# Kernel tuning notes

Measured on AMD Instinct MI355X. Metric: run time of the kernel, lower is better.

Reference implementation:

```python
import jax, jax.numpy as jnp
import numpy as np

LAYER_START = 4
WIN = 2          # context_window_size (over the LAYER axis)
NORM_EPS = 1e-12 # F.normalize eps
COS_EPS = 1e-8   # cosine_similarity eps


def _alpha_for_k(sf, k, nlay):
    """Alignment/novelty weights for layer k. sf: [B, Ttok, Lay, H].
    Mirrors torch: left = tf[k-w:k] (empty when k<w due to python slicing),
    right = tf[k+1:k+w+1], self row last; QR of window_matrix.T."""
    left = list(range(k - WIN, k)) if k >= WIN else []
    right = list(range(k + 1, min(k + WIN + 1, nlay)))
    rows = left + right + [k]
    m = len(rows)  # 3..5
    W = sf[:, :, jnp.array(rows), :]          # [B,T,m,H]
    A = jnp.swapaxes(W, -1, -2)               # [B,T,H,m]  (window_matrix.T)
    _, R = jnp.linalg.qr(A)                   # reduced: R [B,T,m,m]
    r = R[..., :, -1]                         # [B,T,m]
    Rsub = R[..., :-1, :-1]                   # [B,T,m-1,m-1]
    coln = Rsub / jnp.maximum(jnp.linalg.norm(Rsub, axis=-2, keepdims=True), NORM_EPS)
    row_mean = jnp.mean(coln, axis=-1)        # mean over columns -> [B,T,m-1]
    align = jnp.sum(row_mean * R[..., :-1, -1], axis=-1) / jnp.linalg.norm(r[..., :-1], axis=-1)
    align = 1.0 / (align * m * 2)
    novelty = jnp.abs(r[..., -1]) / jnp.linalg.norm(r, axis=-1)
    return align, novelty


def wk_forward(all_hidden_states, attention_mask):
    # [NL,B,T,H] -> [B, Lay, T, H] after layer_start slice
    emb = jnp.transpose(all_hidden_states, (1, 0, 2, 3))[:, LAYER_START:, :, :]
    B, Lay, T, H = emb.shape
    ntok = T - 1  # attention_mask is all-ones: unmask_num = sum(mask) - 1
    sf = jnp.transpose(emb[:, :, :ntok, :], (0, 2, 1, 3))  # [B,Ttok,Lay,H]
    aligns, novs = [], []
    for k in range(Lay):  # small fixed loop over 9 layers
        a, n = _alpha_for_k(sf, k, Lay)
        aligns.append(a)
        novs.append(n)
    align = jnp.stack(aligns, axis=-1)  # [B,Ttok,Lay]
    nov = jnp.stack(novs, axis=-1)
    align = align / jnp.sum(align, axis=-1, keepdims=True)
    nov = nov / jnp.sum(nov, axis=-1, keepdims=True)
    alpha = align + nov
    alpha = alpha / jnp.sum(alpha, axis=-1, keepdims=True)
    token_emb = jnp.einsum('btl,btlh->bth', alpha, sf)  # unify_token output per token
    # unify_sentence: per-token variance (unbiased) of consecutive-layer cosine sims
    a, b = sf[:, :, 1:, :], sf[:, :, :-1, :]
    num = jnp.sum(a * b, axis=-1)
    den = jnp.maximum(jnp.linalg.norm(a, axis=-1) * jnp.linalg.norm(b, axis=-1), COS_EPS)
    sims = num / den                              # [B,Ttok,Lay-1]
    var_tok = jnp.var(sims, axis=-1, ddof=1)      # torch.var default unbiased
    var_tok = var_tok / jnp.sum(var_tok, axis=-1, keepdims=True)
    return jnp.einsum('bt,bth->bh', var_tok, token_emb)  # [B,H]


def setup_inputs() -> dict:
    key = jax.random.key(0)
    NL, B, T, H = 13, 8, 512, 768
    all_hidden_states = jax.random.normal(key, (NL, B, T, H), dtype=jnp.float32)
    attention_mask = jnp.ones((B, T), dtype=jnp.int32)
    return {"all_hidden_states": all_hidden_states, "attention_mask": attention_mask}


def reference(all_hidden_states, attention_mask):
    return wk_forward(all_hidden_states, attention_mask)
```

## Files before the change

kernel.cpp:

```cpp
#include <hip/hip_runtime.h>
#include <math.h>

#define B_DIM 8
#define T_DIM 512
#define H_DIM 768
#define NTOK 511
#define NLAY 9
#define LAYER_START 4
#define NBAND 35
#define TCHUNK 128

__device__ float g_part[B_DIM * TCHUNK * H_DIM];
__device__ float g_varp[B_DIM * TCHUNK];

#define BOFF(d) ((d)*9 - (d) * ((d)-1) / 2)

__global__ __launch_bounds__(256, 4) void wk_a(const float* __restrict__ ahs) {
  const int chunk = blockIdx.x;
  const int b = blockIdx.y;
  const int wave = threadIdx.x >> 6;
  const int lane = threadIdx.x & 63;
  const int t_raw = chunk * 4 + wave;
  const bool active = (t_raw < NTOK);
  const int t = active ? t_raw : (NTOK - 1);

  __shared__ float sG[4][36];
  __shared__ float lds_out[4][H_DIM];
  __shared__ float lds_var[4];

  const size_t LSTR = (size_t)B_DIM * T_DIM * H_DIM;
  const float* lay0 =
      ahs + (size_t)LAYER_START * LSTR + ((size_t)b * T_DIM + t) * H_DIM;

  float g[NBAND];
#pragma unroll
  for (int p = 0; p < NBAND; ++p) g[p] = 0.f;

#pragma unroll 1
  for (int s = 0; s < 3; ++s) {
    const float* p0 = lay0 + s * 256 + lane * 4;
    float4 vs[NLAY];
#pragma unroll
    for (int l = 0; l < NLAY; ++l)
      vs[l] = *reinterpret_cast<const float4*>(p0 + (size_t)l * LSTR);
#pragma unroll
    for (int d = 0; d <= 4; ++d) {
#pragma unroll
      for (int i = 0; i + d < NLAY; ++i) {
        const float4 x = vs[i], y = vs[i + d];
        g[BOFF(d) + i] += x.x * y.x + x.y * y.y + x.z * y.z + x.w * y.w;
      }
    }
  }

#pragma unroll
  for (int off = 32; off > 0; off >>= 1) {
#pragma unroll
    for (int p = 0; p < NBAND; ++p) g[p] += __shfl_xor(g[p], off, 64);
  }

  if (lane == 0) {
#pragma unroll
    for (int p = 0; p < NBAND; ++p) sG[wave][p] = g[p];
  }
  __syncthreads();

  const int k = lane < NLAY ? lane : NLAY - 1;
  const int nl = (k >= 2) ? 2 : 0;
  const int nrr = (NLAY - 1 - k) < 2 ? (NLAY - 1 - k) : 2;
  const int m = nl + nrr + 1;

  auto rowf = [&](int i) -> int {
    return (i < nl) ? (k - 2 + i) : ((i < nl + nrr) ? (k + 1 + i - nl) : k);
  };
  auto GK = [&](int i, int j) -> float {
    int a = rowf(i), c = rowf(j);
    int lo = a < c ? a : c;
    int d = (a < c ? c : a) - lo;
    return sG[wave][d * 9 - d * (d - 1) / 2 + lo];
  };

  float R[5][5];
#pragma unroll
  for (int j = 0; j < 5; ++j)
#pragma unroll
    for (int i = 0; i < 5; ++i) R[i][j] = 0.f;

#pragma unroll
  for (int j = 0; j < 5; ++j) {
    if (j < m) {
#pragma unroll
      for (int i = 0; i < 5; ++i) {
        if (i < j) {
          float s = GK(i, j);
#pragma unroll
          for (int p = 0; p < 4; ++p)
            if (p < i) s -= R[p][i] * R[p][j];
          R[i][j] = s / R[i][i];
        }
      }
      float sjj = GK(j, j);
#pragma unroll
      for (int p = 0; p < 4; ++p)
        if (p < j) sjj -= R[p][j] * R[p][j];
      R[j][j] = sqrtf(fmaxf(sjj, 0.f));
    }
  }

  float r[5];
#pragma unroll
  for (int i = 0; i < 5; ++i)
    r[i] = (m == 3) ? R[i][2] : ((m == 4) ? R[i][3] : R[i][4]);

  float rowmean[4] = {0.f, 0.f, 0.f, 0.f};
#pragma unroll
  for (int j = 0; j < 4; ++j) {
    if (j < m - 1) {
      float cn = 0.f;
#pragma unroll
      for (int i = 0; i < 4; ++i)
        if (i <= j) cn += R[i][j] * R[i][j];
      cn = fmaxf(sqrtf(cn), 1e-12f);
      float inv = 1.f / cn;
#pragma unroll
      for (int i = 0; i < 4; ++i)
        if (i < m - 1) rowmean[i] += R[i][j] * inv;
    }
  }

  const float inv_m1 = 1.f / (float)(m - 1);
  float dotv = 0.f, nrm2 = 0.f;
#pragma unroll
  for (int i = 0; i < 4; ++i) {
    if (i < m - 1) {
      dotv += (rowmean[i] * inv_m1) * r[i];
      nrm2 += r[i] * r[i];
    }
  }
  float align_raw = dotv / sqrtf(nrm2);
  float align_v = 1.f / (align_raw * (float)m * 2.f);
  float rlast = (m == 3) ? r[2] : ((m == 4) ? r[3] : r[4]);
  float nov_v = fabsf(rlast) / sqrtf(nrm2 + rlast * rlast);

  float al[NLAY], nv[NLAY];
  float asum = 0.f, nsum = 0.f;
#pragma unroll
  for (int l = 0; l < NLAY; ++l) {
    al[l] = __shfl(align_v, l, 64);
    nv[l] = __shfl(nov_v, l, 64);
    asum += al[l];
    nsum += nv[l];
  }
  float alpha[NLAY];
  float csum = 0.f;
#pragma unroll
  for (int l = 0; l < NLAY; ++l) {
    alpha[l] = al[l] / asum + nv[l] / nsum;
    csum += alpha[l];
  }
  const float inv_csum = 1.f / csum;

  float sims[NLAY - 1];
  float smean = 0.f;
#pragma unroll
  for (int j = 0; j < NLAY - 1; ++j) {
    float num = sG[wave][BOFF(1) + j];
    float den = fmaxf(sqrtf(sG[wave][j]) * sqrtf(sG[wave][j + 1]), 1e-8f);
    sims[j] = num / den;
    smean += sims[j];
  }
  smean *= (1.f / 8.f);
  float var = 0.f;
#pragma unroll
  for (int j = 0; j < NLAY - 1; ++j) {
    float d = sims[j] - smean;
    var += d * d;
  }
  var *= (1.f / 7.f);
  if (!active) var = 0.f;

  if (lane == 0) lds_var[wave] = var;

  float c[NLAY];
#pragma unroll
  for (int l = 0; l < NLAY; ++l) c[l] = var * alpha[l] * inv_csum;

#pragma unroll 1
  for (int s = 0; s < 3; ++s) {
    const float* p0 = lay0 + s * 256 + lane * 4;
    float4 o;
    o.x = 0.f; o.y = 0.f; o.z = 0.f; o.w = 0.f;
#pragma unroll
    for (int l = 0; l < NLAY; ++l) {
      const float4 vv = *reinterpret_cast<const float4*>(p0 + (size_t)l * LSTR);
      o.x += c[l] * vv.x;
      o.y += c[l] * vv.y;
      o.z += c[l] * vv.z;
      o.w += c[l] * vv.w;
    }
    *reinterpret_cast<float4*>(&lds_out[wave][s * 256 + lane * 4]) = o;
  }
  __syncthreads();

  float* dst = g_part + ((size_t)(b * TCHUNK + chunk)) * H_DIM;
#pragma unroll
  for (int s = 0; s < 3; ++s) {
    int h = s * 256 + threadIdx.x;
    float sum = lds_out[0][h] + lds_out[1][h] + lds_out[2][h] + lds_out[3][h];
    dst[h] = sum;
  }
  if (threadIdx.x == 0) {
    g_varp[b * TCHUNK + chunk] =
        lds_var[0] + lds_var[1] + lds_var[2] + lds_var[3];
  }
}

__global__ __launch_bounds__(256) void wk_r(float* __restrict__ out) {
  const int b = blockIdx.y;
  const int h = blockIdx.x * 256 + threadIdx.x;

  float acc = 0.f;
#pragma unroll 8
  for (int j = 0; j < TCHUNK; ++j)
    acc += g_part[((size_t)(b * TCHUNK + j)) * H_DIM + h];

  float ssum = 0.f;
#pragma unroll 8
  for (int j = 0; j < TCHUNK; ++j) ssum += g_varp[b * TCHUNK + j];

  out[b * H_DIM + h] = acc / ssum;
}

extern "C" void kernel_launch(void* const* d_in, const int* in_sizes, int n_in,
                              void* d_out, int out_size, void* d_ws, size_t ws_size,
                              hipStream_t stream) {
  const float* ahs = (const float*)d_in[0];
  float* out = (float*)d_out;
  (void)d_ws; (void)ws_size;

  wk_a<<<dim3(TCHUNK, B_DIM), dim3(256), 0, stream>>>(ahs);
  wk_r<<<dim3(3, B_DIM), dim3(256), 0, stream>>>(out);
}
```

Before: 241.0 us.

## Keep all layer vectors in registers and reduce Gram bands with DPP

Loads all nine layers' 768-float token slices into registers once (27 float4 per lane) and reuses them for both the Gram computation and the weighted sum, removing the second global read pass. Replaces the 35-value shuffle-xor butterfly with DPP row/bcast reductions, with the result read from lane 63. Occupancy hint drops from 4 to 2 blocks per CU to fit the larger register footprint, trading latency hiding for halved global traffic.

```diff
diff --git a/kernel.cpp b/kernel.cpp
--- a/kernel.cpp
+++ b/kernel.cpp
@@ -15,7 +15,24 @@
 
 #define BOFF(d) ((d)*9 - (d) * ((d)-1) / 2)
 
-__global__ __launch_bounds__(256, 4) void wk_a(const float* __restrict__ ahs) {
+template <int CTRL>
+__device__ __forceinline__ float dpp_mov(float x) {
+  return __builtin_bit_cast(
+      float, __builtin_amdgcn_update_dpp(0, __builtin_bit_cast(int, x), CTRL,
+                                         0xF, 0xF, true));
+}
+
+__device__ __forceinline__ float wave_sum_dpp(float x) {
+  x += dpp_mov<0x111>(x);
+  x += dpp_mov<0x112>(x);
+  x += dpp_mov<0x114>(x);
+  x += dpp_mov<0x118>(x);
+  x += dpp_mov<0x142>(x);
+  x += dpp_mov<0x143>(x);
+  return x;
+}
+
+__global__ __launch_bounds__(256, 2) void wk_a(const float* __restrict__ ahs) {
   const int chunk = blockIdx.x;
   const int b = blockIdx.y;
   const int wave = threadIdx.x >> 6;
@@ -32,34 +49,35 @@
   const float* lay0 =
       ahs + (size_t)LAYER_START * LSTR + ((size_t)b * T_DIM + t) * H_DIM;
 
+  float4 v[NLAY][3];
+#pragma unroll
+  for (int l = 0; l < NLAY; ++l) {
+    const float* base = lay0 + (size_t)l * LSTR;
+#pragma unroll
+    for (int s = 0; s < 3; ++s) {
+      v[l][s] = *reinterpret_cast<const float4*>(base + s * 256 + lane * 4);
+    }
+  }
+
   float g[NBAND];
 #pragma unroll
-  for (int p = 0; p < NBAND; ++p) g[p] = 0.f;
-
-#pragma unroll 1
-  for (int s = 0; s < 3; ++s) {
-    const float* p0 = lay0 + s * 256 + lane * 4;
-    float4 vs[NLAY];
-#pragma unroll
-    for (int l = 0; l < NLAY; ++l)
-      vs[l] = *reinterpret_cast<const float4*>(p0 + (size_t)l * LSTR);
-#pragma unroll
-    for (int d = 0; d <= 4; ++d) {
-#pragma unroll
-      for (int i = 0; i + d < NLAY; ++i) {
-        const float4 x = vs[i], y = vs[i + d];
-        g[BOFF(d) + i] += x.x * y.x + x.y * y.y + x.z * y.z + x.w * y.w;
+  for (int d = 0; d <= 4; ++d) {
+#pragma unroll
+    for (int i = 0; i + d < NLAY; ++i) {
+      float s0 = 0.f;
+#pragma unroll
+      for (int s = 0; s < 3; ++s) {
+        const float4 x = v[i][s], y = v[i + d][s];
+        s0 += x.x * y.x + x.y * y.y + x.z * y.z + x.w * y.w;
       }
-    }
-  }
-
-#pragma unroll
-  for (int off = 32; off > 0; off >>= 1) {
-#pragma unroll
-    for (int p = 0; p < NBAND; ++p) g[p] += __shfl_xor(g[p], off, 64);
-  }
-
-  if (lane == 0) {
+      g[BOFF(d) + i] = s0;
+    }
+  }
+
+#pragma unroll
+  for (int p = 0; p < NBAND; ++p) g[p] = wave_sum_dpp(g[p]);
+
+  if (lane == 63) {
 #pragma unroll
     for (int p = 0; p < NBAND; ++p) sG[wave][p] = g[p];
   }
@@ -185,18 +203,16 @@
 #pragma unroll
   for (int l = 0; l < NLAY; ++l) c[l] = var * alpha[l] * inv_csum;
 
-#pragma unroll 1
+#pragma unroll
   for (int s = 0; s < 3; ++s) {
-    const float* p0 = lay0 + s * 256 + lane * 4;
     float4 o;
     o.x = 0.f; o.y = 0.f; o.z = 0.f; o.w = 0.f;
 #pragma unroll
     for (int l = 0; l < NLAY; ++l) {
-      const float4 vv = *reinterpret_cast<const float4*>(p0 + (size_t)l * LSTR);
-      o.x += c[l] * vv.x;
-      o.y += c[l] * vv.y;
-      o.z += c[l] * vv.z;
-      o.w += c[l] * vv.w;
+      o.x += c[l] * v[l][s].x;
+      o.y += c[l] * v[l][s].y;
+      o.z += c[l] * v[l][s].z;
+      o.w += c[l] * v[l][s].w;
     }
     *reinterpret_cast<float4*>(&lds_out[wave][s * 256 + lane * 4]) = o;
   }
```

Result: faster. 227.2 us (-5.7%).
